# Kernel tuning notes

Hardware: AMD Instinct MI355X
Metric: run time of the kernel (lower is better)

## Reference

```python
import jax, jax.numpy as jnp
import numpy as np

WIN = 11
SIGMA = 1.5
C1 = 0.01 ** 2
C2 = 0.03 ** 2

def _gaussian_window(channel):
    x = np.arange(WIN)
    g = np.exp(-((x - WIN // 2) ** 2) / (2.0 * SIGMA ** 2))
    g = g / g.sum()
    w2d = np.outer(g, g).astype(np.float32)  # [11,11]
    # depthwise kernel: [C, 1, 11, 11] in OIHW with feature_group_count=C
    return jnp.asarray(np.broadcast_to(w2d, (channel, 1, WIN, WIN)).copy())

def _dwconv(x, w, channel):
    pad = WIN // 2
    return jax.lax.conv_general_dilated(
        x, w, window_strides=(1, 1), padding=[(pad, pad), (pad, pad)],
        dimension_numbers=('NCHW', 'OIHW', 'NCHW'),
        feature_group_count=channel)

def _ssim(img1, img2, window, channel):
    mu1 = _dwconv(img1, window, channel)
    mu2 = _dwconv(img2, window, channel)
    mu1_sq = mu1 * mu1
    mu2_sq = mu2 * mu2
    mu1_mu2 = mu1 * mu2
    sigma1_sq = _dwconv(img1 * img1, window, channel) - mu1_sq
    sigma2_sq = _dwconv(img2 * img2, window, channel) - mu2_sq
    sigma12 = _dwconv(img1 * img2, window, channel) - mu1_mu2
    ssim_map = ((2 * mu1_mu2 + C1) * (2 * sigma12 + C2)) / (
        (mu1_sq + mu2_sq + C1) * (sigma1_sq + sigma2_sq + C2))
    return ssim_map.mean()

def setup_inputs() -> dict:
    key = jax.random.key(0)
    kA, kB, kF = jax.random.split(key, 3)
    shape = (16, 3, 512, 512)
    return {
        'image_A': jax.random.uniform(kA, shape, dtype=jnp.float32),
        'image_B': jax.random.uniform(kB, shape, dtype=jnp.float32),
        'image_fused': jax.random.uniform(kF, shape, dtype=jnp.float32),
    }

def reference(image_A, image_B, image_fused):
    channel = image_A.shape[1]
    window = _gaussian_window(channel).astype(image_A.dtype)
    loss = 0.5 * _ssim(image_A, image_fused, window, channel) \
         + 0.5 * _ssim(image_B, image_fused, window, channel)
    return loss
```

## Files before the change

kernel.cpp:

```cpp
#include <hip/hip_runtime.h>
#include <math.h>

#define IMG_W 512
#define IMG_H 512
#define NPLANES 48
#define RROWS 64
#define NCHUNK 8
#define NSTRIP 8
#define WPB 4
#define NGROUP (NCHUNK / WPB)
#define NBLOCKS (NPLANES * NSTRIP * NGROUP)
#define NPAIRS (RROWS / 2 + 5)
#define SSIM_C1 1e-4f
#define SSIM_C2 9e-4f

typedef float f32x2 __attribute__((ext_vector_type(2)));
typedef float f32x4 __attribute__((ext_vector_type(4)));

struct GW { float g[11]; };

__device__ __forceinline__ f32x2 splat2(float v) { return (f32x2){v, v}; }
__device__ __forceinline__ f32x2 fma2(f32x2 a, f32x2 b, f32x2 c) {
  return __builtin_elementwise_fma(a, b, c);
}

__device__ __forceinline__ f32x2 fdiv_fast2(f32x2 n, f32x2 d) {
  f32x2 r = { __builtin_amdgcn_rcpf(d.x), __builtin_amdgcn_rcpf(d.y) };
  r = r * fma2(-d, r, splat2(2.0f));
  f32x2 q = n * r;
  q = fma2(fma2(-d, q, n), r, q);
  return q;
}

#define LDS_ORDER_FENCE() asm volatile("" ::: "memory")

__global__ __launch_bounds__(256, 2) void ssim_main(
    const float* __restrict__ A, const float* __restrict__ B,
    const float* __restrict__ F, double* __restrict__ partials, GW gw)
{
  __shared__ f32x4 sAB[WPB][2][80];
  __shared__ f32x2 sFF[WPB][2][80];
  __shared__ double sred[WPB];
  const int b = blockIdx.x;
  const int plane = b / (NSTRIP * NGROUP);
  const int rem   = b % (NSTRIP * NGROUP);
  const int strip = rem / NGROUP;
  const int grp   = rem % NGROUP;
  const int wid = threadIdx.x >> 6;
  const int t   = threadIdx.x & 63;
  const int chunk = grp * WPB + wid;
  const int x0 = strip * 64;
  const int y0 = chunk * RROWS;
  const size_t pbase = (size_t)plane * (IMG_W * IMG_H);
  const float* Ap = A + pbase;
  const float* Bp = B + pbase;
  const float* Fp = F + pbase;

  f32x4 (&mAB)[2][80] = sAB[wid];
  f32x2 (&mFF)[2][80] = sFF[wid];

  const int c  = x0 - 5 + t;
  const bool cok = (c >= 0) && (c < IMG_W);
  const int c2 = c + 64;
  const bool c2ok = (t < 10) && (c2 < IMG_W);

  f32x2 ring[7][6];
  #pragma unroll
  for (int s = 0; s < 7; ++s)
    #pragma unroll
    for (int k = 0; k < 6; ++k) ring[s][k] = splat2(0.f);

  float acc = 0.f;

  float rA0,rB0,rF0,xA0,xB0,xF0, rA1,rB1,rF1,xA1,xB1,xF1;
  auto load_pair = [&](int ii) {
    const int yin0 = y0 - 5 + 2*ii;
    const int yin1 = yin0 + 1;
    const bool r0 = (yin0 >= 0) && (yin0 < IMG_H);
    const bool r1 = (yin1 >= 0) && (yin1 < IMG_H);
    const size_t o0 = (size_t)yin0 * IMG_W;
    const size_t o1 = (size_t)yin1 * IMG_W;
    rA0 = (r0 && cok) ? Ap[o0 + c] : 0.f;
    rB0 = (r0 && cok) ? Bp[o0 + c] : 0.f;
    rF0 = (r0 && cok) ? Fp[o0 + c] : 0.f;
    rA1 = (r1 && cok) ? Ap[o1 + c] : 0.f;
    rB1 = (r1 && cok) ? Bp[o1 + c] : 0.f;
    rF1 = (r1 && cok) ? Fp[o1 + c] : 0.f;
    xA0 = (r0 && c2ok) ? Ap[o0 + c2] : 0.f;
    xB0 = (r0 && c2ok) ? Bp[o0 + c2] : 0.f;
    xF0 = (r0 && c2ok) ? Fp[o0 + c2] : 0.f;
    xA1 = (r1 && c2ok) ? Ap[o1 + c2] : 0.f;
    xB1 = (r1 && c2ok) ? Bp[o1 + c2] : 0.f;
    xF1 = (r1 && c2ok) ? Fp[o1 + c2] : 0.f;
  };

  load_pair(0);

  for (int jj = 0; jj < 7; ++jj) {
    #pragma unroll
    for (int ph = 0; ph < 6; ++ph) {
      const int ii = jj * 6 + ph;
      if (ii < NPAIRS) {
        const int buf = ii & 1;
        mAB[buf][t] = (f32x4){rA0, rA1, rB0, rB1};
        mFF[buf][t] = (f32x2){rF0, rF1};
        if (t < 10) {
          mAB[buf][t+64] = (f32x4){xA0, xA1, xB0, xB1};
          mFF[buf][t+64] = (f32x2){xF0, xF1};
        }
        LDS_ORDER_FENCE();
        if (ii < NPAIRS - 1) load_pair(ii + 1);
        f32x2 hA=splat2(0.f), hB=splat2(0.f), hF=splat2(0.f),
              hA2=splat2(0.f), hB2=splat2(0.f), hF2=splat2(0.f),
              hAF=splat2(0.f), hBF=splat2(0.f);
        #pragma unroll
        for (int k = 0; k < 11; ++k) {
          const float w = gw.g[k];
          const f32x4 ab = mAB[buf][t+k];
          const f32x2 f  = mFF[buf][t+k];
          const f32x2 a  = {ab.x, ab.y};
          const f32x2 bb = {ab.z, ab.w};
          const f32x2 wv = splat2(w);
          const f32x2 wa = wv*a, wb = wv*bb, wf = wv*f;
          hA += wa; hB += wb; hF += wf;
          hA2 = fma2(wa, a, hA2); hB2 = fma2(wb, bb, hB2); hF2 = fma2(wf, f, hF2);
          hAF = fma2(wa, f, hAF); hBF = fma2(wb, f, hBF);
        }
        ring[0][ph]=hA;  ring[1][ph]=hB;  ring[2][ph]=hF;
        ring[3][ph]=hA2+hF2;  ring[4][ph]=hB2+hF2;
        ring[5][ph]=hAF; ring[6][ph]=hBF;

        if (ii >= 5) {
          f32x2 M[7];
          #pragma unroll
          for (int s = 0; s < 7; ++s) M[s] = splat2(0.f);
          #pragma unroll
          for (int k = 0; k < 11; ++k) {
            const float w = gw.g[k];
            if ((k & 1) == 0) {
              const int p = (ph + 1 + (k >> 1)) % 6;
              const f32x2 wv = splat2(w);
              #pragma unroll
              for (int s = 0; s < 7; ++s) M[s] = fma2(wv, ring[s][p], M[s]);
            } else {
              const int plo = (ph + 1 + (k >> 1)) % 6;
              const int phi = (plo + 1) % 6;
              #pragma unroll
              for (int s = 0; s < 7; ++s) {
                M[s].x = fmaf(w, ring[s][plo].y, M[s].x);
                M[s].y = fmaf(w, ring[s][phi].x, M[s].y);
              }
            }
          }
          const f32x2 mAv=M[0], mBv=M[1], mFv=M[2];
          const f32x2 vS1=M[3], vS2=M[4], vAF=M[5], vBF=M[6];
          const f32x2 mA2=mAv*mAv, mB2=mBv*mBv, mF2=mFv*mFv,
                      mAF=mAv*mFv, mBF=mBv*mFv;
          const f32x2 sAFv = vAF - mAF, sBFv = vBF - mBF;
          const f32x2 ts1 = vS1 - mA2 - mF2;
          const f32x2 ts2 = vS2 - mB2 - mF2;
          const f32x2 two = splat2(2.f), c1 = splat2(SSIM_C1), c2v = splat2(SSIM_C2);
          const f32x2 n1 = fma2(two, mAF, c1) * fma2(two, sAFv, c2v);
          const f32x2 d1 = (mA2 + mF2 + c1) * (ts1 + c2v);
          const f32x2 n2 = fma2(two, mBF, c1) * fma2(two, sBFv, c2v);
          const f32x2 d2 = (mB2 + mF2 + c1) * (ts2 + c2v);
          const f32x2 q1 = fdiv_fast2(n1, d1);
          const f32x2 q2 = fdiv_fast2(n2, d2);
          acc += q1.x + q2.x;
          acc += q1.y + q2.y;
        }
      }
    }
  }

  float wsum = acc;
  #pragma unroll
  for (int off = 32; off > 0; off >>= 1)
    wsum += __shfl_down(wsum, off, 64);
  if (t == 0) sred[wid] = (double)wsum;
  __syncthreads();
  if (threadIdx.x == 0)
    partials[b] = sred[0] + sred[1] + sred[2] + sred[3];
}

__global__ __launch_bounds__(256) void ssim_final(
    const double* __restrict__ partials, float* __restrict__ out)
{
  __shared__ double sd[256];
  const int t = threadIdx.x;
  double s = 0.0;
  for (int i = t; i < NBLOCKS; i += 256) s += partials[i];
  sd[t] = s;
  __syncthreads();
  for (int off = 128; off > 0; off >>= 1) {
    if (t < off) sd[t] += sd[t + off];
    __syncthreads();
  }
  if (t == 0)
    out[0] = (float)(0.5 * sd[0] / (double)(16.0 * 3.0 * 512.0 * 512.0));
}

extern "C" void kernel_launch(void* const* d_in, const int* in_sizes, int n_in,
                              void* d_out, int out_size, void* d_ws, size_t ws_size,
                              hipStream_t stream) {
  const float* A = (const float*)d_in[0];
  const float* B = (const float*)d_in[1];
  const float* F = (const float*)d_in[2];
  double* partials = (double*)d_ws;

  GW gw;
  double g[11], s = 0.0;
  for (int i = 0; i < 11; ++i) { g[i] = exp(-((double)((i-5)*(i-5))) / 4.5); s += g[i]; }
  for (int i = 0; i < 11; ++i) gw.g[i] = (float)(g[i] / s);

  hipLaunchKernelGGL(ssim_main, dim3(NBLOCKS), dim3(WPB * 64), 0, stream,
                     A, B, F, partials, gw);
  hipLaunchKernelGGL(ssim_final, dim3(1), dim3(256), 0, stream,
                     partials, (float*)d_out);
}
```

Measured before the change: 198.7 us.

## Deepen global-load prefetch to three row pairs with register triple buffering

Global loads are now issued three row-pairs ahead instead of one, into a three-slot register buffer. Each iteration writes the next pair into the alternate LDS buffer before the horizontal pass reads the current one. The aim is to hide more global memory latency behind the horizontal and vertical convolution math. The cost is about 24 more live VGPRs per thread, which could hurt occupancy or cause spills under the launch bound of 2 blocks.

```diff
diff --git a/kernel.cpp b/kernel.cpp
--- a/kernel.cpp
+++ b/kernel.cpp
@@ -72,52 +72,67 @@
 
   float acc = 0.f;
 
-  float rA0,rB0,rF0,xA0,xB0,xF0, rA1,rB1,rF1,xA1,xB1,xF1;
-  auto load_pair = [&](int ii) {
+  float rA0[3],rA1[3],rB0[3],rB1[3],rF0[3],rF1[3];
+  float xA0[3],xA1[3],xB0[3],xB1[3],xF0[3],xF1[3];
+  auto load_pair = [&](int ii, int set) {
     const int yin0 = y0 - 5 + 2*ii;
     const int yin1 = yin0 + 1;
     const bool r0 = (yin0 >= 0) && (yin0 < IMG_H);
     const bool r1 = (yin1 >= 0) && (yin1 < IMG_H);
     const size_t o0 = (size_t)yin0 * IMG_W;
     const size_t o1 = (size_t)yin1 * IMG_W;
-    rA0 = (r0 && cok) ? Ap[o0 + c] : 0.f;
-    rB0 = (r0 && cok) ? Bp[o0 + c] : 0.f;
-    rF0 = (r0 && cok) ? Fp[o0 + c] : 0.f;
-    rA1 = (r1 && cok) ? Ap[o1 + c] : 0.f;
-    rB1 = (r1 && cok) ? Bp[o1 + c] : 0.f;
-    rF1 = (r1 && cok) ? Fp[o1 + c] : 0.f;
-    xA0 = (r0 && c2ok) ? Ap[o0 + c2] : 0.f;
-    xB0 = (r0 && c2ok) ? Bp[o0 + c2] : 0.f;
-    xF0 = (r0 && c2ok) ? Fp[o0 + c2] : 0.f;
-    xA1 = (r1 && c2ok) ? Ap[o1 + c2] : 0.f;
-    xB1 = (r1 && c2ok) ? Bp[o1 + c2] : 0.f;
-    xF1 = (r1 && c2ok) ? Fp[o1 + c2] : 0.f;
+    rA0[set] = (r0 && cok) ? Ap[o0 + c] : 0.f;
+    rB0[set] = (r0 && cok) ? Bp[o0 + c] : 0.f;
+    rF0[set] = (r0 && cok) ? Fp[o0 + c] : 0.f;
+    rA1[set] = (r1 && cok) ? Ap[o1 + c] : 0.f;
+    rB1[set] = (r1 && cok) ? Bp[o1 + c] : 0.f;
+    rF1[set] = (r1 && cok) ? Fp[o1 + c] : 0.f;
+    xA0[set] = (r0 && c2ok) ? Ap[o0 + c2] : 0.f;
+    xB0[set] = (r0 && c2ok) ? Bp[o0 + c2] : 0.f;
+    xF0[set] = (r0 && c2ok) ? Fp[o0 + c2] : 0.f;
+    xA1[set] = (r1 && c2ok) ? Ap[o1 + c2] : 0.f;
+    xB1[set] = (r1 && c2ok) ? Bp[o1 + c2] : 0.f;
+    xF1[set] = (r1 && c2ok) ? Fp[o1 + c2] : 0.f;
   };
 
-  load_pair(0);
+  load_pair(0, 0);
+  load_pair(1, 1);
+  load_pair(2, 2);
+  mAB[0][t] = (f32x4){rA0[0], rA1[0], rB0[0], rB1[0]};
+  mFF[0][t] = (f32x2){rF0[0], rF1[0]};
+  if (t < 10) {
+    mAB[0][t+64] = (f32x4){xA0[0], xA1[0], xB0[0], xB1[0]};
+    mFF[0][t+64] = (f32x2){xF0[0], xF1[0]};
+  }
 
   for (int jj = 0; jj < 7; ++jj) {
     #pragma unroll
     for (int ph = 0; ph < 6; ++ph) {
       const int ii = jj * 6 + ph;
       if (ii < NPAIRS) {
-        const int buf = ii & 1;
-        mAB[buf][t] = (f32x4){rA0, rA1, rB0, rB1};
-        mFF[buf][t] = (f32x2){rF0, rF1};
-        if (t < 10) {
-          mAB[buf][t+64] = (f32x4){xA0, xA1, xB0, xB1};
-          mFF[buf][t+64] = (f32x2){xF0, xF1};
+        const int rbuf = ph & 1;
+        const int wbuf = (ph + 1) & 1;
+        const int sst  = (ph + 1) % 3;
+        const int sld  = ph % 3;
+        LDS_ORDER_FENCE();
+        if (ii + 1 < NPAIRS) {
+          mAB[wbuf][t] = (f32x4){rA0[sst], rA1[sst], rB0[sst], rB1[sst]};
+          mFF[wbuf][t] = (f32x2){rF0[sst], rF1[sst]};
+          if (t < 10) {
+            mAB[wbuf][t+64] = (f32x4){xA0[sst], xA1[sst], xB0[sst], xB1[sst]};
+            mFF[wbuf][t+64] = (f32x2){xF0[sst], xF1[sst]};
+          }
         }
+        if (ii + 3 < NPAIRS) load_pair(ii + 3, sld);
         LDS_ORDER_FENCE();
-        if (ii < NPAIRS - 1) load_pair(ii + 1);
         f32x2 hA=splat2(0.f), hB=splat2(0.f), hF=splat2(0.f),
               hA2=splat2(0.f), hB2=splat2(0.f), hF2=splat2(0.f),
               hAF=splat2(0.f), hBF=splat2(0.f);
         #pragma unroll
         for (int k = 0; k < 11; ++k) {
           const float w = gw.g[k];
-          const f32x4 ab = mAB[buf][t+k];
-          const f32x2 f  = mFF[buf][t+k];
+          const f32x4 ab = mAB[rbuf][t+k];
+          const f32x2 f  = mFF[rbuf][t+k];
           const f32x2 a  = {ab.x, ab.y};
           const f32x2 bb = {ab.z, ab.w};
           const f32x2 wv = splat2(w);
```

Result: no change. 201.0 us (+1.2%).
